# Kernel tuning notes

Measured on AMD Instinct MI355X. Metric: run time of the kernel, lower is better.

The kernel has to match this reference:

```python
import jax, jax.numpy as jnp
import numpy as np

L = 5          # num_layer
H = 32         # num_heads (feature dim)
G = 32         # n_graph
NN = 256       # n_node per graph
KB = 8         # adjacency band half-width
N = G * (2 * (KB * NN - KB * (KB + 1) // 2))   # 128768 angle-graph nodes
E = N * 16                                      # 2060288 angle-graph edges
NRBF = 20
BN_EPS = 1e-5
GAMMA = 10.0


def _band_adj():
    i = np.arange(NN)
    d = np.abs(i[:, None] - i[None, :])
    a = (d <= KB) & (d > 0)
    return jnp.asarray(np.broadcast_to(a, (G, NN, NN)).copy())


def setup_inputs() -> dict:
    key = jax.random.key(0)
    ks = jax.random.split(key, 10)
    adj = _band_adj()
    x_mask = jnp.ones((G, NN), dtype=bool)
    x_3d = jax.random.uniform(ks[0], (N, 1), minval=0.8, maxval=1.8)
    edge_attr_3d = jax.random.uniform(ks[1], (E, 1), minval=0.0, maxval=float(np.pi))
    edge_index = jax.random.randint(ks[2], (2, E), 0, N)
    s1 = 1.0 / np.sqrt(NRBF)
    sH = 1.0 / np.sqrt(H)
    s2H = 1.0 / np.sqrt(2 * H)
    return {
        "x_3d": x_3d, "edge_attr_3d": edge_attr_3d,
        "edge_index": edge_index, "adj": adj, "x_mask": x_mask,
        "w_len": jax.random.normal(ks[3], (NRBF, H)) * s1, "b_len": jnp.zeros(H),
        "w_ang": jax.random.normal(ks[4], (NRBF, H)) * s1, "b_ang": jnp.zeros(H),
        "w1": jax.random.normal(ks[5], (L, H, 2 * H)) * sH, "b1": jnp.zeros((L, 2 * H)),
        "bn1_g": jnp.ones((L, 2 * H)), "bn1_b": jnp.zeros((L, 2 * H)),
        "w2": jax.random.normal(ks[6], (L, 2 * H, H)) * s2H, "b2": jnp.zeros((L, H)),
        "eps_gin": jnp.zeros(L),
        "bn_g": jnp.ones((L, H)), "bn_b": jnp.zeros((L, H)),
        "ln_g": jnp.ones(H), "ln_b": jnp.zeros(H),
    }


def _bn(h, g, b):
    # BatchNorm1d in training mode (batch statistics)
    m = jnp.mean(h, axis=0)
    v = jnp.var(h, axis=0)
    return (h - m) * jax.lax.rsqrt(v + BN_EPS) * g + b


def _rbf(x, centers):
    # x: [M,1] -> [M, NRBF]
    return jnp.exp(-GAMMA * (x - centers) ** 2)


def _forward(x_3d, edge_attr_3d, edge_index, adj,
             w_len, b_len, w_ang, b_ang,
             w1, b1, bn1_g, bn1_b, w2, b2, eps_gin, bn_g, bn_b, ln_g, ln_b):
    cen_len = jnp.arange(NRBF, dtype=x_3d.dtype) * 0.1           # bond length RBF centers
    cen_ang = jnp.linspace(0.0, np.pi, NRBF).astype(x_3d.dtype)  # bond angle RBF centers
    x = _rbf(x_3d, cen_len) @ w_len + b_len                      # [N,H]
    ea = _rbf(edge_attr_3d, cen_ang) @ w_ang + b_ang             # [E,H]
    src, dst = edge_index[0], edge_index[1]

    h = x
    for l in range(L):
        # GINConvBondAngle: message = relu(x_j + edge_attr); aggr = add
        msg = jax.nn.relu(h[src] + ea)                           # [E,H]
        agg = jax.ops.segment_sum(msg, dst, num_segments=N)      # [N,H]
        z = (1.0 + eps_gin[l]) * h + agg
        z = _bn(z @ w1[l] + b1[l], bn1_g[l], bn1_b[l])           # mlp Linear+BN
        z = jax.nn.relu(z) @ w2[l] + b2[l]                       # mlp ReLU+Linear
        h = _bn(z, bn_g[l], bn_b[l])                             # outer batch norm
        if l != L - 1:
            h = jax.nn.relu(h)
        # dropout p=0 -> identity; residual=False; JK='last'

    mu = jnp.mean(h, axis=-1, keepdims=True)
    var = jnp.var(h, axis=-1, keepdims=True)
    nr = (h - mu) * jax.lax.rsqrt(var + BN_EPS) * ln_g + ln_b    # LayerNorm, [N,H]

    # masked dense scatter into [G*NN*NN, H]
    eye = jnp.eye(NN, dtype=bool)
    mask = (adj & ~eye).reshape(-1)                              # exactly N Trues
    pos = jnp.cumsum(mask) - 1                                   # row in nr for each True
    out = jnp.where(mask[:, None], nr[jnp.clip(pos, 0, N - 1)], 0.0)
    return out.reshape(G, NN, NN, H).transpose(0, 3, 1, 2)       # [G,H,NN,NN]


def reference(x_3d, edge_attr_3d, edge_index, adj, x_mask,
              w_len, b_len, w_ang, b_ang,
              w1, b1, bn1_g, bn1_b, w2, b2, eps_gin, bn_g, bn_b, ln_g, ln_b):
    return _forward(x_3d, edge_attr_3d, edge_index, adj,
                    w_len, b_len, w_ang, b_ang,
                    w1, b1, bn1_g, bn1_b, w2, b2, eps_gin, bn_g, bn_b, ln_g, ln_b)
```

## Files before the change

kernel.cpp:

```cpp
#include <hip/hip_runtime.h>
#include <hip/hip_bf16.h>
#include <hip/hip_fp16.h>

#define HH 32
#define HH2 64
#define NRBF_ 20
#define NL 5
#define NNN 256
#define KBW 8
#define PGN 4024
#define TTAB 4096
constexpr int NNODE = 128768;
constexpr int NEDGE = 2060288;
constexpr float BNEPS = 1e-5f;
constexpr float PI_F = 3.14159265358979323846f;

__global__ void __launch_bounds__(256) k_node_embed(const float* __restrict__ x3d,
                                                    const float* __restrict__ wlen,
                                                    const float* __restrict__ blen,
                                                    __half* __restrict__ hbuf) {
  __shared__ float wl[NRBF_ * HH];
  __shared__ float bl[HH];
  int t = threadIdx.x;
  for (int j = t; j < NRBF_ * HH; j += 256) wl[j] = wlen[j];
  if (t < HH) bl[t] = blen[t];
  __syncthreads();
  int idx = blockIdx.x * 256 + t;
  int n = idx >> 5, c = idx & 31;
  float x = x3d[n];
  float acc = bl[c];
#pragma unroll
  for (int k = 0; k < NRBF_; ++k) {
    float d = x - 0.1f * (float)k;
    acc = fmaf(__expf(-10.f * d * d), wl[k * HH + c], acc);
  }
  hbuf[idx] = __float2half(acc);
}

__global__ void __launch_bounds__(256) k_tab(const float* __restrict__ wang,
                                             const float* __restrict__ bang,
                                             __half* __restrict__ tab) {
  __shared__ float wa[NRBF_ * HH];
  __shared__ float ba[HH];
  int t = threadIdx.x;
  for (int j = t; j < NRBF_ * HH; j += 256) wa[j] = wang[j];
  if (t < HH) ba[t] = bang[t];
  __syncthreads();
  int idx = blockIdx.x * 256 + t;
  int row = idx >> 5, c = idx & 31;
  float ang = (float)row * (PI_F / (float)(TTAB - 1));
  const float step = PI_F / 19.f;
  float acc = ba[c];
#pragma unroll
  for (int k = 0; k < NRBF_; ++k) {
    float d = ang - step * (float)k;
    acc = fmaf(__expf(-10.f * d * d), wa[k * HH + c], acc);
  }
  tab[row * HH + c] = __float2half(acc);
}

__global__ void __launch_bounds__(256) k_hist(const int* __restrict__ dst, int* __restrict__ counts) {
  int e = blockIdx.x * 256 + threadIdx.x;
  atomicAdd(&counts[dst[e]], 1);
}

__global__ void __launch_bounds__(256) k_scan1(const int* __restrict__ counts, int* __restrict__ bsum) {
  __shared__ int sd[256];
  int t = threadIdx.x;
  sd[t] = counts[blockIdx.x * 256 + t];
  __syncthreads();
  for (int s = 128; s > 0; s >>= 1) { if (t < s) sd[t] += sd[t + s]; __syncthreads(); }
  if (t == 0) bsum[blockIdx.x] = sd[0];
}

__global__ void __launch_bounds__(512) k_scan2(const int* __restrict__ bsum, int* __restrict__ boff) {
  __shared__ int sd[512];
  int t = threadIdx.x;
  int v = (t < 503) ? bsum[t] : 0;
  sd[t] = v;
  __syncthreads();
  for (int off = 1; off < 512; off <<= 1) {
    int x = (t >= off) ? sd[t - off] : 0;
    __syncthreads();
    sd[t] += x;
    __syncthreads();
  }
  if (t < 503) boff[t] = sd[t] - v;
}

__global__ void __launch_bounds__(256) k_scan3(const int* __restrict__ counts, const int* __restrict__ boff,
                                               int* __restrict__ rowptr, int* __restrict__ cursor) {
  __shared__ int sd[256];
  int t = threadIdx.x;
  int i = blockIdx.x * 256 + t;
  int v = counts[i];
  sd[t] = v;
  __syncthreads();
  for (int off = 1; off < 256; off <<= 1) {
    int x = (t >= off) ? sd[t - off] : 0;
    __syncthreads();
    sd[t] += x;
    __syncthreads();
  }
  int excl = sd[t] - v + boff[blockIdx.x];
  rowptr[i] = excl;
  cursor[i] = excl;
  if (i == NNODE - 1) rowptr[NNODE] = excl + v;
}

__global__ void __launch_bounds__(256) k_scatter(const int* __restrict__ srcA,
                                                 const int* __restrict__ dstA,
                                                 const float* __restrict__ eattr,
                                                 int* __restrict__ cursor,
                                                 unsigned int* __restrict__ pk) {
  const float angsc = (float)(TTAB - 1) / PI_F;
  int bid = blockIdx.x;
  int x = bid & 7;
  int j = bid >> 3;
  int lo = x * (NNODE / 8);
  int hi = lo + (NNODE / 8);
  int e0 = j * 2048 + threadIdx.x;
#pragma unroll
  for (int k = 0; k < 8; ++k) {
    int e = e0 + k * 256;
    int d = dstA[e];
    if (d >= lo && d < hi) {
      int pos = atomicAdd(&cursor[d], 1);
      unsigned int idx = min((unsigned int)fmaf(eattr[e], angsc, 0.5f), (unsigned int)(TTAB - 1));
      pk[pos] = (unsigned int)srcA[e] | (idx << 17);
    }
  }
}

__global__ void __launch_bounds__(256) k_layerA(const __half* __restrict__ hbuf,
                                                const int* __restrict__ rowptr,
                                                const unsigned int* __restrict__ pk,
                                                const __half* __restrict__ tab,
                                                const float* __restrict__ statsC,
                                                const float* __restrict__ bng,
                                                const float* __restrict__ bnb,
                                                const float* __restrict__ w1g,
                                                const float* __restrict__ b1g,
                                                const float* __restrict__ epsg,
                                                __half* __restrict__ y1buf,
                                                float* __restrict__ statsA,
                                                int l, int relu) {
  __shared__ float w1s[HH * HH2];
  __shared__ float b1s[HH2];
  __shared__ float affs[HH], affsh[HH];
  __shared__ float tb[8][HH + 1];
  __shared__ float ps[HH2], pq[HH2];
  int t = threadIdx.x;
  const float* w1l = w1g + l * HH * HH2;
  for (int j = t; j < HH * HH2; j += 256) w1s[j] = w1l[j];
  if (t < HH2) { b1s[t] = b1g[l * HH2 + t]; ps[t] = 0.f; pq[t] = 0.f; }
  if (t < HH) {
    if (l == 0) { affs[t] = 1.f; affsh[t] = 0.f; }
    else {
      float sum = statsC[(l - 1) * 64 + t], sq = statsC[(l - 1) * 64 + 32 + t];
      float mean = sum / (float)NNODE;
      float var = fmaxf(sq / (float)NNODE - mean * mean, 0.f);
      float s = bng[(l - 1) * HH + t] * rsqrtf(var + BNEPS);
      affs[t] = s; affsh[t] = bnb[(l - 1) * HH + t] - mean * s;
    }
  }
  int g = t >> 5, c = t & 31;
  float epsv = 1.f + epsg[l];
  float lo = relu ? 0.f : -3.4e38f;
  float s0a = 0.f, s0q = 0.f, s1a = 0.f, s1q = 0.f;
  __syncthreads();
  float sc = affs[c], sh = affsh[c];
  int stride = gridDim.x * 8;
  int iters = (NNODE + stride - 1) / stride;
  int n = blockIdx.x * 8 + g;
  for (int it = 0; it < iters; ++it, n += stride) {
    bool val = n < NNODE;
    float tv = 0.f;
    if (val) {
      int p0 = rowptr[n], p1 = rowptr[n + 1];
      float hn = fmaxf(fmaf(__half2float(hbuf[n * HH + c]), sc, sh), lo);
      float acc = 0.f;
      int p = p0;
      for (; p + 8 <= p1; p += 8) {
        unsigned int q0 = __builtin_nontemporal_load(&pk[p]);
        unsigned int q1 = __builtin_nontemporal_load(&pk[p + 1]);
        unsigned int q2 = __builtin_nontemporal_load(&pk[p + 2]);
        unsigned int q3 = __builtin_nontemporal_load(&pk[p + 3]);
        unsigned int q4 = __builtin_nontemporal_load(&pk[p + 4]);
        unsigned int q5 = __builtin_nontemporal_load(&pk[p + 5]);
        unsigned int q6 = __builtin_nontemporal_load(&pk[p + 6]);
        unsigned int q7 = __builtin_nontemporal_load(&pk[p + 7]);
        float h0 = __half2float(hbuf[(q0 & 0x1FFFF) * HH + c]);
        float h1 = __half2float(hbuf[(q1 & 0x1FFFF) * HH + c]);
        float h2 = __half2float(hbuf[(q2 & 0x1FFFF) * HH + c]);
        float h3 = __half2float(hbuf[(q3 & 0x1FFFF) * HH + c]);
        float h4 = __half2float(hbuf[(q4 & 0x1FFFF) * HH + c]);
        float h5 = __half2float(hbuf[(q5 & 0x1FFFF) * HH + c]);
        float h6 = __half2float(hbuf[(q6 & 0x1FFFF) * HH + c]);
        float h7 = __half2float(hbuf[(q7 & 0x1FFFF) * HH + c]);
        float e0 = __half2float(tab[(q0 >> 17) * HH + c]);
        float e1 = __half2float(tab[(q1 >> 17) * HH + c]);
        float e2 = __half2float(tab[(q2 >> 17) * HH + c]);
        float e3 = __half2float(tab[(q3 >> 17) * HH + c]);
        float e4 = __half2float(tab[(q4 >> 17) * HH + c]);
        float e5 = __half2float(tab[(q5 >> 17) * HH + c]);
        float e6 = __half2float(tab[(q6 >> 17) * HH + c]);
        float e7 = __half2float(tab[(q7 >> 17) * HH + c]);
        h0 = fmaxf(fmaf(h0, sc, sh), lo); h1 = fmaxf(fmaf(h1, sc, sh), lo);
        h2 = fmaxf(fmaf(h2, sc, sh), lo); h3 = fmaxf(fmaf(h3, sc, sh), lo);
        h4 = fmaxf(fmaf(h4, sc, sh), lo); h5 = fmaxf(fmaf(h5, sc, sh), lo);
        h6 = fmaxf(fmaf(h6, sc, sh), lo); h7 = fmaxf(fmaf(h7, sc, sh), lo);
        acc += fmaxf(h0 + e0, 0.f) + fmaxf(h1 + e1, 0.f) + fmaxf(h2 + e2, 0.f) + fmaxf(h3 + e3, 0.f)
             + fmaxf(h4 + e4, 0.f) + fmaxf(h5 + e5, 0.f) + fmaxf(h6 + e6, 0.f) + fmaxf(h7 + e7, 0.f);
      }
      for (; p < p1; ++p) {
        unsigned int q0 = __builtin_nontemporal_load(&pk[p]);
        float h0 = fmaxf(fmaf(__half2float(hbuf[(q0 & 0x1FFFF) * HH + c]), sc, sh), lo);
        acc += fmaxf(h0 + __half2float(tab[(q0 >> 17) * HH + c]), 0.f);
      }
      tv = fmaf(epsv, hn, acc);
    }
    tb[g][c] = tv;
    __builtin_amdgcn_wave_barrier();
    if (val) {
      float y0 = b1s[c], y1 = b1s[HH + c];
#pragma unroll
      for (int k = 0; k < HH; ++k) {
        float tk = tb[g][k];
        y0 = fmaf(tk, w1s[k * HH2 + c], y0);
        y1 = fmaf(tk, w1s[k * HH2 + HH + c], y1);
      }
      __half hy0 = __float2half(y0), hy1 = __float2half(y1);
      y1buf[n * HH2 + c] = hy0;
      y1buf[n * HH2 + HH + c] = hy1;
      float z0 = __half2float(hy0), z1 = __half2float(hy1);
      s0a += z0; s0q += z0 * z0; s1a += z1; s1q += z1 * z1;
    }
    __builtin_amdgcn_wave_barrier();
  }
  s0a += __shfl_xor(s0a, 32); s0q += __shfl_xor(s0q, 32);
  s1a += __shfl_xor(s1a, 32); s1q += __shfl_xor(s1q, 32);
  if ((t & 32) == 0) {
    atomicAdd(&ps[c], s0a); atomicAdd(&pq[c], s0q);
    atomicAdd(&ps[HH + c], s1a); atomicAdd(&pq[HH + c], s1q);
  }
  __syncthreads();
  if (t < HH2) {
    atomicAdd(&statsA[l * 128 + t], ps[t]);
    atomicAdd(&statsA[l * 128 + 64 + t], pq[t]);
  }
}

__global__ void __launch_bounds__(256) k_layerC(const __half* __restrict__ y1buf,
                                                const float* __restrict__ statsA,
                                                const float* __restrict__ g1,
                                                const float* __restrict__ bb1,
                                                const float* __restrict__ w2g,
                                                const float* __restrict__ b2g,
                                                __half* __restrict__ hbuf,
                                                float* __restrict__ statsC, int l) {
  __shared__ float w2s[HH2 * HH];
  __shared__ float b2s[HH];
  __shared__ float a1s[HH2], a1sh[HH2];
  __shared__ float ab[8][HH2 + 1];
  __shared__ float ps[HH], pq[HH];
  int t = threadIdx.x;
  const float* w2l = w2g + l * HH2 * HH;
  for (int j = t; j < HH2 * HH; j += 256) w2s[j] = w2l[j];
  if (t < HH) { b2s[t] = b2g[l * HH + t]; ps[t] = 0.f; pq[t] = 0.f; }
  if (t < HH2) {
    float sum = statsA[l * 128 + t], sq = statsA[l * 128 + 64 + t];
    float mean = sum / (float)NNODE;
    float var = fmaxf(sq / (float)NNODE - mean * mean, 0.f);
    float s = g1[l * HH2 + t] * rsqrtf(var + BNEPS);
    a1s[t] = s; a1sh[t] = bb1[l * HH2 + t] - mean * s;
  }
  int g = t >> 5, c = t & 31;
  float sa = 0.f, sq = 0.f;
  __syncthreads();
  int stride = gridDim.x * 8;
  int iters = (NNODE + stride - 1) / stride;
  int n = blockIdx.x * 8 + g;
  for (int it = 0; it < iters; ++it, n += stride) {
    bool val = n < NNODE;
    float a0 = 0.f, a1 = 0.f;
    if (val) {
      a0 = fmaf(__half2float(y1buf[n * HH2 + c]), a1s[c], a1sh[c]);
      a1 = fmaf(__half2float(y1buf[n * HH2 + HH + c]), a1s[HH + c], a1sh[HH + c]);
    }
    ab[g][c] = fmaxf(a0, 0.f);
    ab[g][HH + c] = fmaxf(a1, 0.f);
    __builtin_amdgcn_wave_barrier();
    if (val) {
      float z = b2s[c];
#pragma unroll
      for (int k = 0; k < HH2; ++k) z = fmaf(ab[g][k], w2s[k * HH + c], z);
      __half zh = __float2half(z);
      hbuf[n * HH + c] = zh;
      float zq = __half2float(zh);
      sa += zq; sq += zq * zq;
    }
    __builtin_amdgcn_wave_barrier();
  }
  sa += __shfl_xor(sa, 32); sq += __shfl_xor(sq, 32);
  if ((t & 32) == 0) { atomicAdd(&ps[c], sa); atomicAdd(&pq[c], sq); }
  __syncthreads();
  if (t < HH) {
    atomicAdd(&statsC[l * 64 + t], ps[t]);
    atomicAdd(&statsC[l * 64 + 32 + t], pq[t]);
  }
}

__global__ void __launch_bounds__(256) k_output(const __half* __restrict__ hbuf,
                                                const float* __restrict__ statsC,
                                                const float* __restrict__ bng,
                                                const float* __restrict__ bnb,
                                                const float* __restrict__ lng,
                                                const float* __restrict__ lnb,
                                                float* __restrict__ out) {
  __shared__ float nrb[16 * 33];
  __shared__ float affs[HH], affsh[HH];
  int t = threadIdx.x;
  if (t < HH) {
    float sum = statsC[(NL - 1) * 64 + t], sq = statsC[(NL - 1) * 64 + 32 + t];
    float mean = sum / (float)NNODE;
    float var = fmaxf(sq / (float)NNODE - mean * mean, 0.f);
    float s = bng[(NL - 1) * HH + t] * rsqrtf(var + BNEPS);
    affs[t] = s; affsh[t] = bnb[(NL - 1) * HH + t] - mean * s;
  }
  __syncthreads();
  int gi = blockIdx.x;
  int g = gi >> 8, i = gi & 255;
  int jlo = (i - KBW > 0) ? i - KBW : 0;
  int jhi = (i + KBW < NNN - 1) ? i + KBW : NNN - 1;
  int cnt = jhi - jlo;
  int Ai = (i <= 8) ? i * (i - 1) / 2 : 28 + 8 * (i - 8);
  int Bi = (i <= 248) ? 8 * i : 2012 - (256 - i) * (255 - i) / 2;
  int nb = g * PGN + Ai + Bi;
  int r = t >> 5, c = t & 31;
  float sc = affs[c], sh = affsh[c];
  float lg = lng[c], lb = lnb[c];
  for (int rr = r; rr < cnt; rr += 8) {
    float v = fmaf(__half2float(hbuf[(nb + rr) * HH + c]), sc, sh);
    float s = v;
#pragma unroll
    for (int off = 16; off > 0; off >>= 1) s += __shfl_xor(s, off, 32);
    float mean = s * (1.f / 32.f);
    float d = v - mean;
    float q = d * d;
#pragma unroll
    for (int off = 16; off > 0; off >>= 1) q += __shfl_xor(q, off, 32);
    float var = q * (1.f / 32.f);
    nrb[rr * 33 + c] = d * rsqrtf(var + BNEPS) * lg + lb;
  }
  __syncthreads();
  int j = t;
  bool valid = (j >= jlo) & (j <= jhi) & (j != i);
  int rr = j - jlo - ((j > i) ? 1 : 0);
  rr = (rr < 0) ? 0 : ((rr > 15) ? 15 : rr);
  size_t ob = (((size_t)g * HH) * NNN + i) * NNN + j;
#pragma unroll
  for (int h = 0; h < HH; ++h) {
    float val = valid ? nrb[rr * 33 + h] : 0.f;
    __builtin_nontemporal_store(val, &out[ob + (size_t)h * NNN * NNN]);
  }
}

extern "C" void kernel_launch(void* const* d_in, const int* in_sizes, int n_in,
                              void* d_out, int out_size, void* d_ws, size_t ws_size,
                              hipStream_t stream) {
  (void)in_sizes; (void)n_in;
  const float* x3d   = (const float*)d_in[0];
  const float* eattr = (const float*)d_in[1];
  const int*   eidx  = (const int*)d_in[2];
  const float* wlen = (const float*)d_in[5];
  const float* blen = (const float*)d_in[6];
  const float* wang = (const float*)d_in[7];
  const float* bang = (const float*)d_in[8];
  const float* w1g  = (const float*)d_in[9];
  const float* b1g  = (const float*)d_in[10];
  const float* g1   = (const float*)d_in[11];
  const float* bb1  = (const float*)d_in[12];
  const float* w2g  = (const float*)d_in[13];
  const float* b2g  = (const float*)d_in[14];
  const float* epsg = (const float*)d_in[15];
  const float* bng  = (const float*)d_in[16];
  const float* bnb  = (const float*)d_in[17];
  const float* lng  = (const float*)d_in[18];
  const float* lnb  = (const float*)d_in[19];
  float* out = (float*)d_out;

  char* ws = (char*)d_ws;
  size_t off = 0;
  auto alloc = [&](size_t bytes) {
    void* p = ws + off;
    off += (bytes + 255) & ~(size_t)255;
    return p;
  };
  unsigned int* pk  = (unsigned int*)alloc((size_t)NEDGE * 4);
  int*   rowptr     = (int*)alloc((size_t)(NNODE + 1) * 4);
  int*   counts     = (int*)alloc((size_t)NNODE * 4);
  int*   cursor     = (int*)alloc((size_t)NNODE * 4);
  __half* hbuf      = (__half*)alloc((size_t)NNODE * HH * 2);
  __half* y1buf     = (__half*)alloc((size_t)NNODE * HH2 * 2);
  __half* tab       = (__half*)alloc((size_t)TTAB * HH * 2);
  float* statsA     = (float*)alloc(NL * 128 * 4);
  float* statsC     = (float*)alloc(NL * 64 * 4);
  int*   bsum       = (int*)alloc(503 * 4);
  int*   boff       = (int*)alloc(503 * 4);

  if (off > ws_size) {
    hipMemsetAsync(d_out, 0x7F, (size_t)out_size * 4, stream);
    return;
  }

  hipMemsetAsync(counts, 0, (size_t)NNODE * 4, stream);
  hipMemsetAsync(statsA, 0, NL * 128 * 4, stream);
  hipMemsetAsync(statsC, 0, NL * 64 * 4, stream);

  k_node_embed<<<NNODE * HH / 256, 256, 0, stream>>>(x3d, wlen, blen, hbuf);
  k_tab<<<TTAB * HH / 256, 256, 0, stream>>>(wang, bang, tab);
  k_hist<<<NEDGE / 256, 256, 0, stream>>>(eidx + NEDGE, counts);
  k_scan1<<<NNODE / 256, 256, 0, stream>>>(counts, bsum);
  k_scan2<<<1, 512, 0, stream>>>(bsum, boff);
  k_scan3<<<NNODE / 256, 256, 0, stream>>>(counts, boff, rowptr, cursor);
  k_scatter<<<8048, 256, 0, stream>>>(eidx, eidx + NEDGE, eattr, cursor, pk);

  for (int l = 0; l < NL; ++l) {
    k_layerA<<<2048, 256, 0, stream>>>(hbuf, rowptr, pk, tab, statsC, bng, bnb,
                                       w1g, b1g, epsg, y1buf, statsA, l, l >= 1 ? 1 : 0);
    k_layerC<<<2048, 256, 0, stream>>>(y1buf, statsA, g1, bb1, w2g, b2g, hbuf, statsC, l);
  }

  k_output<<<NNN * 32, 256, 0, stream>>>(hbuf, statsC, bng, bnb, lng, lnb, out);
}
```

Before: 1.144 ms.

## Map one wavefront per node, split edges across half-waves, merge prep kernels

Layer kernels now give each 64-lane wavefront one node instead of a 32-lane half-wave. The gather splits the edge list between the two halves and combines them with a cross-lane shuffle. The per-node matvecs now use all 64 lanes (one output per lane in layerA, split-K with a shuffle reduce in layerC). The embedding, angle-table and histogram kernels are merged into one launch, and the two stats memsets are combined. This is meant to raise memory-level parallelism per node and cut launch overhead, but it halves the nodes in flight per block and adds shuffle work.

```diff
diff --git a/kernel.cpp b/kernel.cpp
--- a/kernel.cpp
+++ b/kernel.cpp
@@ -15,53 +15,58 @@
 constexpr float BNEPS = 1e-5f;
 constexpr float PI_F = 3.14159265358979323846f;
 
-__global__ void __launch_bounds__(256) k_node_embed(const float* __restrict__ x3d,
-                                                    const float* __restrict__ wlen,
-                                                    const float* __restrict__ blen,
-                                                    __half* __restrict__ hbuf) {
-  __shared__ float wl[NRBF_ * HH];
-  __shared__ float bl[HH];
-  int t = threadIdx.x;
-  for (int j = t; j < NRBF_ * HH; j += 256) wl[j] = wlen[j];
-  if (t < HH) bl[t] = blen[t];
-  __syncthreads();
-  int idx = blockIdx.x * 256 + t;
-  int n = idx >> 5, c = idx & 31;
-  float x = x3d[n];
-  float acc = bl[c];
-#pragma unroll
-  for (int k = 0; k < NRBF_; ++k) {
-    float d = x - 0.1f * (float)k;
-    acc = fmaf(__expf(-10.f * d * d), wl[k * HH + c], acc);
-  }
-  hbuf[idx] = __float2half(acc);
-}
-
-__global__ void __launch_bounds__(256) k_tab(const float* __restrict__ wang,
-                                             const float* __restrict__ bang,
-                                             __half* __restrict__ tab) {
-  __shared__ float wa[NRBF_ * HH];
-  __shared__ float ba[HH];
-  int t = threadIdx.x;
-  for (int j = t; j < NRBF_ * HH; j += 256) wa[j] = wang[j];
-  if (t < HH) ba[t] = bang[t];
-  __syncthreads();
-  int idx = blockIdx.x * 256 + t;
-  int row = idx >> 5, c = idx & 31;
-  float ang = (float)row * (PI_F / (float)(TTAB - 1));
-  const float step = PI_F / 19.f;
-  float acc = ba[c];
-#pragma unroll
-  for (int k = 0; k < NRBF_; ++k) {
-    float d = ang - step * (float)k;
-    acc = fmaf(__expf(-10.f * d * d), wa[k * HH + c], acc);
-  }
-  tab[row * HH + c] = __float2half(acc);
-}
-
-__global__ void __launch_bounds__(256) k_hist(const int* __restrict__ dst, int* __restrict__ counts) {
-  int e = blockIdx.x * 256 + threadIdx.x;
-  atomicAdd(&counts[dst[e]], 1);
+#define EMB_BLKS (NNODE * HH / 256)
+#define TAB_BLKS (TTAB * HH / 256)
+#define HIST_BLKS (NEDGE / 256)
+
+__global__ void __launch_bounds__(256) k_prep(const float* __restrict__ x3d,
+                                              const float* __restrict__ wlen,
+                                              const float* __restrict__ blen,
+                                              const float* __restrict__ wang,
+                                              const float* __restrict__ bang,
+                                              const int* __restrict__ dst,
+                                              __half* __restrict__ hbuf,
+                                              __half* __restrict__ tab,
+                                              int* __restrict__ counts) {
+  int b = blockIdx.x;
+  int t = threadIdx.x;
+  if (b < EMB_BLKS) {
+    __shared__ float wl[NRBF_ * HH];
+    __shared__ float bl[HH];
+    for (int j = t; j < NRBF_ * HH; j += 256) wl[j] = wlen[j];
+    if (t < HH) bl[t] = blen[t];
+    __syncthreads();
+    int idx = b * 256 + t;
+    int n = idx >> 5, c = idx & 31;
+    float x = x3d[n];
+    float acc = bl[c];
+#pragma unroll
+    for (int k = 0; k < NRBF_; ++k) {
+      float d = x - 0.1f * (float)k;
+      acc = fmaf(__expf(-10.f * d * d), wl[k * HH + c], acc);
+    }
+    hbuf[idx] = __float2half(acc);
+  } else if (b < EMB_BLKS + TAB_BLKS) {
+    __shared__ float wa[NRBF_ * HH];
+    __shared__ float ba[HH];
+    for (int j = t; j < NRBF_ * HH; j += 256) wa[j] = wang[j];
+    if (t < HH) ba[t] = bang[t];
+    __syncthreads();
+    int idx = (b - EMB_BLKS) * 256 + t;
+    int row = idx >> 5, c = idx & 31;
+    float ang = (float)row * (PI_F / (float)(TTAB - 1));
+    const float step = PI_F / 19.f;
+    float acc = ba[c];
+#pragma unroll
+    for (int k = 0; k < NRBF_; ++k) {
+      float d = ang - step * (float)k;
+      acc = fmaf(__expf(-10.f * d * d), wa[k * HH + c], acc);
+    }
+    tab[row * HH + c] = __float2half(acc);
+  } else {
+    int e = (b - EMB_BLKS - TAB_BLKS) * 256 + t;
+    atomicAdd(&counts[dst[e]], 1);
+  }
 }
 
 __global__ void __launch_bounds__(256) k_scan1(const int* __restrict__ counts, int* __restrict__ bsum) {
@@ -148,7 +153,7 @@
   __shared__ float w1s[HH * HH2];
   __shared__ float b1s[HH2];
   __shared__ float affs[HH], affsh[HH];
-  __shared__ float tb[8][HH + 1];
+  __shared__ float tb[4][HH + 1];
   __shared__ float ps[HH2], pq[HH2];
   int t = threadIdx.x;
   const float* w1l = w1g + l * HH * HH2;
@@ -164,32 +169,31 @@
       affs[t] = s; affsh[t] = bnb[(l - 1) * HH + t] - mean * s;
     }
   }
-  int g = t >> 5, c = t & 31;
+  int wave = t >> 6, lane = t & 63, half = lane >> 5, c = lane & 31;
   float epsv = 1.f + epsg[l];
   float lo = relu ? 0.f : -3.4e38f;
-  float s0a = 0.f, s0q = 0.f, s1a = 0.f, s1q = 0.f;
+  float sreg = 0.f, qreg = 0.f;
   __syncthreads();
   float sc = affs[c], sh = affsh[c];
-  int stride = gridDim.x * 8;
+  int stride = gridDim.x * 4;
   int iters = (NNODE + stride - 1) / stride;
-  int n = blockIdx.x * 8 + g;
+  int n = blockIdx.x * 4 + wave;
   for (int it = 0; it < iters; ++it, n += stride) {
     bool val = n < NNODE;
-    float tv = 0.f;
     if (val) {
       int p0 = rowptr[n], p1 = rowptr[n + 1];
       float hn = fmaxf(fmaf(__half2float(hbuf[n * HH + c]), sc, sh), lo);
       float acc = 0.f;
-      int p = p0;
-      for (; p + 8 <= p1; p += 8) {
+      int p = p0 + half;
+      while (p + 14 < p1) {
         unsigned int q0 = __builtin_nontemporal_load(&pk[p]);
-        unsigned int q1 = __builtin_nontemporal_load(&pk[p + 1]);
-        unsigned int q2 = __builtin_nontemporal_load(&pk[p + 2]);
-        unsigned int q3 = __builtin_nontemporal_load(&pk[p + 3]);
-        unsigned int q4 = __builtin_nontemporal_load(&pk[p + 4]);
-        unsigned int q5 = __builtin_nontemporal_load(&pk[p + 5]);
-        unsigned int q6 = __builtin_nontemporal_load(&pk[p + 6]);
-        unsigned int q7 = __builtin_nontemporal_load(&pk[p + 7]);
+        unsigned int q1 = __builtin_nontemporal_load(&pk[p + 2]);
+        unsigned int q2 = __builtin_nontemporal_load(&pk[p + 4]);
+        unsigned int q3 = __builtin_nontemporal_load(&pk[p + 6]);
+        unsigned int q4 = __builtin_nontemporal_load(&pk[p + 8]);
+        unsigned int q5 = __builtin_nontemporal_load(&pk[p + 10]);
+        unsigned int q6 = __builtin_nontemporal_load(&pk[p + 12]);
+        unsigned int q7 = __builtin_nontemporal_load(&pk[p + 14]);
         float h0 = __half2float(hbuf[(q0 & 0x1FFFF) * HH + c]);
         float h1 = __half2float(hbuf[(q1 & 0x1FFFF) * HH + c]);
         float h2 = __half2float(hbuf[(q2 & 0x1FFFF) * HH + c]);
@@ -212,43 +216,35 @@
         h6 = fmaxf(fmaf(h6, sc, sh), lo); h7 = fmaxf(fmaf(h7, sc, sh), lo);
         acc += fmaxf(h0 + e0, 0.f) + fmaxf(h1 + e1, 0.f) + fmaxf(h2 + e2, 0.f) + fmaxf(h3 + e3, 0.f)
              + fmaxf(h4 + e4, 0.f) + fmaxf(h5 + e5, 0.f) + fmaxf(h6 + e6, 0.f) + fmaxf(h7 + e7, 0.f);
+        p += 16;
       }
-      for (; p < p1; ++p) {
+      for (; p < p1; p += 2) {
         unsigned int q0 = __builtin_nontemporal_load(&pk[p]);
         float h0 = fmaxf(fmaf(__half2float(hbuf[(q0 & 0x1FFFF) * HH + c]), sc, sh), lo);
         acc += fmaxf(h0 + __half2float(tab[(q0 >> 17) * HH + c]), 0.f);
       }
-      tv = fmaf(epsv, hn, acc);
-    }
-    tb[g][c] = tv;
+      acc += __shfl_xor(acc, 32);
+      float tv = fmaf(epsv, hn, acc);
+      if (half == 0) tb[wave][c] = tv;
+    }
     __builtin_amdgcn_wave_barrier();
     if (val) {
-      float y0 = b1s[c], y1 = b1s[HH + c];
-#pragma unroll
-      for (int k = 0; k < HH; ++k) {
-        float tk = tb[g][k];
-        y0 = fmaf(tk, w1s[k * HH2 + c], y0);
-        y1 = fmaf(tk, w1s[k * HH2 + HH + c], y1);
-      }
-      __half hy0 = __float2half(y0), hy1 = __float2half(y1);
-      y1buf[n * HH2 + c] = hy0;
-      y1buf[n * HH2 + HH + c] = hy1;
-      float z0 = __half2float(hy0), z1 = __half2float(hy1);
-      s0a += z0; s0q += z0 * z0; s1a += z1; s1q += z1 * z1;
+      float y = b1s[lane];
+#pragma unroll
+      for (int k = 0; k < HH; ++k) y = fmaf(tb[wave][k], w1s[k * HH2 + lane], y);
+      __half hy = __float2half(y);
+      y1buf[n * HH2 + lane] = hy;
+      float z = __half2float(hy);
+      sreg += z; qreg += z * z;
     }
     __builtin_amdgcn_wave_barrier();
   }
-  s0a += __shfl_xor(s0a, 32); s0q += __shfl_xor(s0q, 32);
-  s1a += __shfl_xor(s1a, 32); s1q += __shfl_xor(s1q, 32);
-  if ((t & 32) == 0) {
-    atomicAdd(&ps[c], s0a); atomicAdd(&pq[c], s0q);
-    atomicAdd(&ps[HH + c], s1a); atomicAdd(&pq[HH + c], s1q);
-  }
-  __syncthreads();
-  if (t < HH2) {
-    atomicAdd(&statsA[l * 128 + t], ps[t]);
-    atomicAdd(&statsA[l * 128 + 64 + t], pq[t]);
-  }
+  __syncthreads();
+  atomicAdd(&ps[lane], sreg);
+  atomicAdd(&pq[lane], qreg);
+  __syncthreads();
+  if (t < HH2) atomicAdd(&statsA[l * 128 + t], ps[t]);
+  else if (t < 128) atomicAdd(&statsA[l * 128 + t], pq[t - HH2]);
 }
 
 __global__ void __launch_bounds__(256) k_layerC(const __half* __restrict__ y1buf,
@@ -262,7 +258,7 @@
   __shared__ float w2s[HH2 * HH];
   __shared__ float b2s[HH];
   __shared__ float a1s[HH2], a1sh[HH2];
-  __shared__ float ab[8][HH2 + 1];
+  __shared__ float ab[4][HH2 + 1];
   __shared__ float ps[HH], pq[HH];
   int t = threadIdx.x;
   const float* w2l = w2g + l * HH2 * HH;
@@ -275,40 +271,39 @@
     float s = g1[l * HH2 + t] * rsqrtf(var + BNEPS);
     a1s[t] = s; a1sh[t] = bb1[l * HH2 + t] - mean * s;
   }
-  int g = t >> 5, c = t & 31;
-  float sa = 0.f, sq = 0.f;
-  __syncthreads();
-  int stride = gridDim.x * 8;
+  int wave = t >> 6, lane = t & 63, half = lane >> 5, c = lane & 31;
+  float sreg = 0.f, qreg = 0.f;
+  __syncthreads();
+  int stride = gridDim.x * 4;
   int iters = (NNODE + stride - 1) / stride;
-  int n = blockIdx.x * 8 + g;
+  int n = blockIdx.x * 4 + wave;
   for (int it = 0; it < iters; ++it, n += stride) {
     bool val = n < NNODE;
-    float a0 = 0.f, a1 = 0.f;
     if (val) {
-      a0 = fmaf(__half2float(y1buf[n * HH2 + c]), a1s[c], a1sh[c]);
-      a1 = fmaf(__half2float(y1buf[n * HH2 + HH + c]), a1s[HH + c], a1sh[HH + c]);
-    }
-    ab[g][c] = fmaxf(a0, 0.f);
-    ab[g][HH + c] = fmaxf(a1, 0.f);
+      float a = fmaf(__half2float(y1buf[n * HH2 + lane]), a1s[lane], a1sh[lane]);
+      ab[wave][lane] = fmaxf(a, 0.f);
+    }
     __builtin_amdgcn_wave_barrier();
     if (val) {
-      float z = b2s[c];
-#pragma unroll
-      for (int k = 0; k < HH2; ++k) z = fmaf(ab[g][k], w2s[k * HH + c], z);
-      __half zh = __float2half(z);
-      hbuf[n * HH + c] = zh;
-      float zq = __half2float(zh);
-      sa += zq; sq += zq * zq;
+      float z = (half == 0) ? b2s[c] : 0.f;
+      int kb = half << 5;
+#pragma unroll
+      for (int k2 = 0; k2 < HH; ++k2) z = fmaf(ab[wave][kb + k2], w2s[(kb + k2) * HH + c], z);
+      z += __shfl_xor(z, 32);
+      if (half == 0) {
+        __half zh = __float2half(z);
+        hbuf[n * HH + c] = zh;
+        float zq = __half2float(zh);
+        sreg += zq; qreg += zq * zq;
+      }
     }
     __builtin_amdgcn_wave_barrier();
   }
-  sa += __shfl_xor(sa, 32); sq += __shfl_xor(sq, 32);
-  if ((t & 32) == 0) { atomicAdd(&ps[c], sa); atomicAdd(&pq[c], sq); }
-  __syncthreads();
-  if (t < HH) {
-    atomicAdd(&statsC[l * 64 + t], ps[t]);
-    atomicAdd(&statsC[l * 64 + 32 + t], pq[t]);
-  }
+  __syncthreads();
+  if (half == 0) { atomicAdd(&ps[c], sreg); atomicAdd(&pq[c], qreg); }
+  __syncthreads();
+  if (t < HH) atomicAdd(&statsC[l * 64 + t], ps[t]);
+  else if (t < 64) atomicAdd(&statsC[l * 64 + t], pq[t - HH]);
 }
 
 __global__ void __launch_bounds__(256) k_output(const __half* __restrict__ hbuf,
@@ -404,8 +399,8 @@
   __half* hbuf      = (__half*)alloc((size_t)NNODE * HH * 2);
   __half* y1buf     = (__half*)alloc((size_t)NNODE * HH2 * 2);
   __half* tab       = (__half*)alloc((size_t)TTAB * HH * 2);
-  float* statsA     = (float*)alloc(NL * 128 * 4);
-  float* statsC     = (float*)alloc(NL * 64 * 4);
+  float* statsA     = (float*)alloc((NL * 128 + NL * 64) * 4);
+  float* statsC     = statsA + NL * 128;
   int*   bsum       = (int*)alloc(503 * 4);
   int*   boff       = (int*)alloc(503 * 4);
 
@@ -415,12 +410,10 @@
   }
 
   hipMemsetAsync(counts, 0, (size_t)NNODE * 4, stream);
-  hipMemsetAsync(statsA, 0, NL * 128 * 4, stream);
-  hipMemsetAsync(statsC, 0, NL * 64 * 4, stream);
-
-  k_node_embed<<<NNODE * HH / 256, 256, 0, stream>>>(x3d, wlen, blen, hbuf);
-  k_tab<<<TTAB * HH / 256, 256, 0, stream>>>(wang, bang, tab);
-  k_hist<<<NEDGE / 256, 256, 0, stream>>>(eidx + NEDGE, counts);
+  hipMemsetAsync(statsA, 0, (NL * 128 + NL * 64) * 4, stream);
+
+  k_prep<<<EMB_BLKS + TAB_BLKS + HIST_BLKS, 256, 0, stream>>>(x3d, wlen, blen, wang, bang,
+                                                              eidx + NEDGE, hbuf, tab, counts);
   k_scan1<<<NNODE / 256, 256, 0, stream>>>(counts, bsum);
   k_scan2<<<1, 512, 0, stream>>>(bsum, boff);
   k_scan3<<<NNODE / 256, 256, 0, stream>>>(counts, boff, rowptr, cursor);
```

Result: slower. 1.277 ms (+11.6%).

## Split edge gather into two passes by source-node half for cache locality

Applied to the files above, without the earlier changes.

Edges are bucketed per destination node by whether the source index lies in the lower or upper half of the node range. Each layer now runs two gather kernels, each touching only half of the half-precision feature buffer, so the working set of the random gathers is meant to fit better in cache. In exchange it adds an extra float partial-sum buffer write and read per layer, one extra kernel launch per layer, and a doubled histogram and scan.

```diff
diff --git a/kernel.cpp b/kernel.cpp
--- a/kernel.cpp
+++ b/kernel.cpp
@@ -11,6 +11,8 @@
 #define PGN 4024
 #define TTAB 4096
 constexpr int NNODE = 128768;
+constexpr int NHALF = NNODE / 2;
+constexpr int N2 = NNODE * 2;
 constexpr int NEDGE = 2060288;
 constexpr float BNEPS = 1e-5f;
 constexpr float PI_F = 3.14159265358979323846f;
@@ -59,9 +61,12 @@
   tab[row * HH + c] = __float2half(acc);
 }
 
-__global__ void __launch_bounds__(256) k_hist(const int* __restrict__ dst, int* __restrict__ counts) {
+__global__ void __launch_bounds__(256) k_hist(const int* __restrict__ srcA,
+                                              const int* __restrict__ dstA,
+                                              int* __restrict__ counts) {
   int e = blockIdx.x * 256 + threadIdx.x;
-  atomicAdd(&counts[dst[e]], 1);
+  int bin = dstA[e] * 2 + (srcA[e] >= NHALF ? 1 : 0);
+  atomicAdd(&counts[bin], 1);
 }
 
 __global__ void __launch_bounds__(256) k_scan1(const int* __restrict__ counts, int* __restrict__ bsum) {
@@ -73,23 +78,23 @@
   if (t == 0) bsum[blockIdx.x] = sd[0];
 }
 
-__global__ void __launch_bounds__(512) k_scan2(const int* __restrict__ bsum, int* __restrict__ boff) {
-  __shared__ int sd[512];
-  int t = threadIdx.x;
-  int v = (t < 503) ? bsum[t] : 0;
+__global__ void __launch_bounds__(1024) k_scan2(const int* __restrict__ bsum, int* __restrict__ boff) {
+  __shared__ int sd[1024];
+  int t = threadIdx.x;
+  int v = (t < 1006) ? bsum[t] : 0;
   sd[t] = v;
   __syncthreads();
-  for (int off = 1; off < 512; off <<= 1) {
+  for (int off = 1; off < 1024; off <<= 1) {
     int x = (t >= off) ? sd[t - off] : 0;
     __syncthreads();
     sd[t] += x;
     __syncthreads();
   }
-  if (t < 503) boff[t] = sd[t] - v;
+  if (t < 1006) boff[t] = sd[t] - v;
 }
 
 __global__ void __launch_bounds__(256) k_scan3(const int* __restrict__ counts, const int* __restrict__ boff,
-                                               int* __restrict__ rowptr, int* __restrict__ cursor) {
+                                               int* __restrict__ rowptr2, int* __restrict__ cursor2) {
   __shared__ int sd[256];
   int t = threadIdx.x;
   int i = blockIdx.x * 256 + t;
@@ -103,15 +108,15 @@
     __syncthreads();
   }
   int excl = sd[t] - v + boff[blockIdx.x];
-  rowptr[i] = excl;
-  cursor[i] = excl;
-  if (i == NNODE - 1) rowptr[NNODE] = excl + v;
+  rowptr2[i] = excl;
+  cursor2[i] = excl;
+  if (i == N2 - 1) rowptr2[N2] = excl + v;
 }
 
 __global__ void __launch_bounds__(256) k_scatter(const int* __restrict__ srcA,
                                                  const int* __restrict__ dstA,
                                                  const float* __restrict__ eattr,
-                                                 int* __restrict__ cursor,
+                                                 int* __restrict__ cursor2,
                                                  unsigned int* __restrict__ pk) {
   const float angsc = (float)(TTAB - 1) / PI_F;
   int bid = blockIdx.x;
@@ -125,26 +130,112 @@
     int e = e0 + k * 256;
     int d = dstA[e];
     if (d >= lo && d < hi) {
-      int pos = atomicAdd(&cursor[d], 1);
+      int s = srcA[e];
+      int bin = d * 2 + (s >= NHALF ? 1 : 0);
+      int pos = atomicAdd(&cursor2[bin], 1);
       unsigned int idx = min((unsigned int)fmaf(eattr[e], angsc, 0.5f), (unsigned int)(TTAB - 1));
-      pk[pos] = (unsigned int)srcA[e] | (idx << 17);
-    }
-  }
-}
-
-__global__ void __launch_bounds__(256) k_layerA(const __half* __restrict__ hbuf,
-                                                const int* __restrict__ rowptr,
-                                                const unsigned int* __restrict__ pk,
-                                                const __half* __restrict__ tab,
-                                                const float* __restrict__ statsC,
-                                                const float* __restrict__ bng,
-                                                const float* __restrict__ bnb,
-                                                const float* __restrict__ w1g,
-                                                const float* __restrict__ b1g,
-                                                const float* __restrict__ epsg,
-                                                __half* __restrict__ y1buf,
-                                                float* __restrict__ statsA,
-                                                int l, int relu) {
+      pk[pos] = (unsigned int)s | (idx << 17);
+    }
+  }
+}
+
+__device__ __forceinline__ float edge_gather(const __half* __restrict__ hbuf,
+                                             const __half* __restrict__ tab,
+                                             const unsigned int* __restrict__ pk,
+                                             int p0, int p1, int c,
+                                             float sc, float sh, float lo) {
+  float acc = 0.f;
+  int p = p0;
+  for (; p + 8 <= p1; p += 8) {
+    unsigned int q0 = __builtin_nontemporal_load(&pk[p]);
+    unsigned int q1 = __builtin_nontemporal_load(&pk[p + 1]);
+    unsigned int q2 = __builtin_nontemporal_load(&pk[p + 2]);
+    unsigned int q3 = __builtin_nontemporal_load(&pk[p + 3]);
+    unsigned int q4 = __builtin_nontemporal_load(&pk[p + 4]);
+    unsigned int q5 = __builtin_nontemporal_load(&pk[p + 5]);
+    unsigned int q6 = __builtin_nontemporal_load(&pk[p + 6]);
+    unsigned int q7 = __builtin_nontemporal_load(&pk[p + 7]);
+    float h0 = __half2float(hbuf[(q0 & 0x1FFFF) * HH + c]);
+    float h1 = __half2float(hbuf[(q1 & 0x1FFFF) * HH + c]);
+    float h2 = __half2float(hbuf[(q2 & 0x1FFFF) * HH + c]);
+    float h3 = __half2float(hbuf[(q3 & 0x1FFFF) * HH + c]);
+    float h4 = __half2float(hbuf[(q4 & 0x1FFFF) * HH + c]);
+    float h5 = __half2float(hbuf[(q5 & 0x1FFFF) * HH + c]);
+    float h6 = __half2float(hbuf[(q6 & 0x1FFFF) * HH + c]);
+    float h7 = __half2float(hbuf[(q7 & 0x1FFFF) * HH + c]);
+    float e0 = __half2float(tab[(q0 >> 17) * HH + c]);
+    float e1 = __half2float(tab[(q1 >> 17) * HH + c]);
+    float e2 = __half2float(tab[(q2 >> 17) * HH + c]);
+    float e3 = __half2float(tab[(q3 >> 17) * HH + c]);
+    float e4 = __half2float(tab[(q4 >> 17) * HH + c]);
+    float e5 = __half2float(tab[(q5 >> 17) * HH + c]);
+    float e6 = __half2float(tab[(q6 >> 17) * HH + c]);
+    float e7 = __half2float(tab[(q7 >> 17) * HH + c]);
+    h0 = fmaxf(fmaf(h0, sc, sh), lo); h1 = fmaxf(fmaf(h1, sc, sh), lo);
+    h2 = fmaxf(fmaf(h2, sc, sh), lo); h3 = fmaxf(fmaf(h3, sc, sh), lo);
+    h4 = fmaxf(fmaf(h4, sc, sh), lo); h5 = fmaxf(fmaf(h5, sc, sh), lo);
+    h6 = fmaxf(fmaf(h6, sc, sh), lo); h7 = fmaxf(fmaf(h7, sc, sh), lo);
+    acc += fmaxf(h0 + e0, 0.f) + fmaxf(h1 + e1, 0.f) + fmaxf(h2 + e2, 0.f) + fmaxf(h3 + e3, 0.f)
+         + fmaxf(h4 + e4, 0.f) + fmaxf(h5 + e5, 0.f) + fmaxf(h6 + e6, 0.f) + fmaxf(h7 + e7, 0.f);
+  }
+  for (; p < p1; ++p) {
+    unsigned int q0 = __builtin_nontemporal_load(&pk[p]);
+    float h0 = fmaxf(fmaf(__half2float(hbuf[(q0 & 0x1FFFF) * HH + c]), sc, sh), lo);
+    acc += fmaxf(h0 + __half2float(tab[(q0 >> 17) * HH + c]), 0.f);
+  }
+  return acc;
+}
+
+__global__ void __launch_bounds__(256) k_layerA0(const __half* __restrict__ hbuf,
+                                                 const int* __restrict__ rowptr2,
+                                                 const unsigned int* __restrict__ pk,
+                                                 const __half* __restrict__ tab,
+                                                 const float* __restrict__ statsC,
+                                                 const float* __restrict__ bng,
+                                                 const float* __restrict__ bnb,
+                                                 float* __restrict__ partf,
+                                                 int l, int relu) {
+  __shared__ float affs[HH], affsh[HH];
+  int t = threadIdx.x;
+  if (t < HH) {
+    if (l == 0) { affs[t] = 1.f; affsh[t] = 0.f; }
+    else {
+      float sum = statsC[(l - 1) * 64 + t], sq = statsC[(l - 1) * 64 + 32 + t];
+      float mean = sum / (float)NNODE;
+      float var = fmaxf(sq / (float)NNODE - mean * mean, 0.f);
+      float s = bng[(l - 1) * HH + t] * rsqrtf(var + BNEPS);
+      affs[t] = s; affsh[t] = bnb[(l - 1) * HH + t] - mean * s;
+    }
+  }
+  int g = t >> 5, c = t & 31;
+  float lo = relu ? 0.f : -3.4e38f;
+  __syncthreads();
+  float sc = affs[c], sh = affsh[c];
+  int stride = gridDim.x * 8;
+  int iters = (NNODE + stride - 1) / stride;
+  int n = blockIdx.x * 8 + g;
+  for (int it = 0; it < iters; ++it, n += stride) {
+    if (n < NNODE) {
+      int p0 = rowptr2[2 * n], p1 = rowptr2[2 * n + 1];
+      partf[n * HH + c] = edge_gather(hbuf, tab, pk, p0, p1, c, sc, sh, lo);
+    }
+  }
+}
+
+__global__ void __launch_bounds__(256) k_layerA1(const __half* __restrict__ hbuf,
+                                                 const int* __restrict__ rowptr2,
+                                                 const unsigned int* __restrict__ pk,
+                                                 const __half* __restrict__ tab,
+                                                 const float* __restrict__ partf,
+                                                 const float* __restrict__ statsC,
+                                                 const float* __restrict__ bng,
+                                                 const float* __restrict__ bnb,
+                                                 const float* __restrict__ w1g,
+                                                 const float* __restrict__ b1g,
+                                                 const float* __restrict__ epsg,
+                                                 __half* __restrict__ y1buf,
+                                                 float* __restrict__ statsA,
+                                                 int l, int relu) {
   __shared__ float w1s[HH * HH2];
   __shared__ float b1s[HH2];
   __shared__ float affs[HH], affsh[HH];
@@ -177,47 +268,10 @@
     bool val = n < NNODE;
     float tv = 0.f;
     if (val) {
-      int p0 = rowptr[n], p1 = rowptr[n + 1];
+      int p0 = rowptr2[2 * n + 1], p1 = rowptr2[2 * n + 2];
+      float acc = edge_gather(hbuf, tab, pk, p0, p1, c, sc, sh, lo);
+      acc += partf[n * HH + c];
       float hn = fmaxf(fmaf(__half2float(hbuf[n * HH + c]), sc, sh), lo);
-      float acc = 0.f;
-      int p = p0;
-      for (; p + 8 <= p1; p += 8) {
-        unsigned int q0 = __builtin_nontemporal_load(&pk[p]);
-        unsigned int q1 = __builtin_nontemporal_load(&pk[p + 1]);
-        unsigned int q2 = __builtin_nontemporal_load(&pk[p + 2]);
-        unsigned int q3 = __builtin_nontemporal_load(&pk[p + 3]);
-        unsigned int q4 = __builtin_nontemporal_load(&pk[p + 4]);
-        unsigned int q5 = __builtin_nontemporal_load(&pk[p + 5]);
-        unsigned int q6 = __builtin_nontemporal_load(&pk[p + 6]);
-        unsigned int q7 = __builtin_nontemporal_load(&pk[p + 7]);
-        float h0 = __half2float(hbuf[(q0 & 0x1FFFF) * HH + c]);
-        float h1 = __half2float(hbuf[(q1 & 0x1FFFF) * HH + c]);
-        float h2 = __half2float(hbuf[(q2 & 0x1FFFF) * HH + c]);
-        float h3 = __half2float(hbuf[(q3 & 0x1FFFF) * HH + c]);
-        float h4 = __half2float(hbuf[(q4 & 0x1FFFF) * HH + c]);
-        float h5 = __half2float(hbuf[(q5 & 0x1FFFF) * HH + c]);
-        float h6 = __half2float(hbuf[(q6 & 0x1FFFF) * HH + c]);
-        float h7 = __half2float(hbuf[(q7 & 0x1FFFF) * HH + c]);
-        float e0 = __half2float(tab[(q0 >> 17) * HH + c]);
-        float e1 = __half2float(tab[(q1 >> 17) * HH + c]);
-        float e2 = __half2float(tab[(q2 >> 17) * HH + c]);
-        float e3 = __half2float(tab[(q3 >> 17) * HH + c]);
-        float e4 = __half2float(tab[(q4 >> 17) * HH + c]);
-        float e5 = __half2float(tab[(q5 >> 17) * HH + c]);
-        float e6 = __half2float(tab[(q6 >> 17) * HH + c]);
-        float e7 = __half2float(tab[(q7 >> 17) * HH + c]);
-        h0 = fmaxf(fmaf(h0, sc, sh), lo); h1 = fmaxf(fmaf(h1, sc, sh), lo);
-        h2 = fmaxf(fmaf(h2, sc, sh), lo); h3 = fmaxf(fmaf(h3, sc, sh), lo);
-        h4 = fmaxf(fmaf(h4, sc, sh), lo); h5 = fmaxf(fmaf(h5, sc, sh), lo);
-        h6 = fmaxf(fmaf(h6, sc, sh), lo); h7 = fmaxf(fmaf(h7, sc, sh), lo);
-        acc += fmaxf(h0 + e0, 0.f) + fmaxf(h1 + e1, 0.f) + fmaxf(h2 + e2, 0.f) + fmaxf(h3 + e3, 0.f)
-             + fmaxf(h4 + e4, 0.f) + fmaxf(h5 + e5, 0.f) + fmaxf(h6 + e6, 0.f) + fmaxf(h7 + e7, 0.f);
-      }
-      for (; p < p1; ++p) {
-        unsigned int q0 = __builtin_nontemporal_load(&pk[p]);
-        float h0 = fmaxf(fmaf(__half2float(hbuf[(q0 & 0x1FFFF) * HH + c]), sc, sh), lo);
-        acc += fmaxf(h0 + __half2float(tab[(q0 >> 17) * HH + c]), 0.f);
-      }
       tv = fmaf(epsv, hn, acc);
     }
     tb[g][c] = tv;
@@ -398,37 +452,39 @@
     return p;
   };
   unsigned int* pk  = (unsigned int*)alloc((size_t)NEDGE * 4);
-  int*   rowptr     = (int*)alloc((size_t)(NNODE + 1) * 4);
-  int*   counts     = (int*)alloc((size_t)NNODE * 4);
-  int*   cursor     = (int*)alloc((size_t)NNODE * 4);
+  int*   rowptr2    = (int*)alloc((size_t)(N2 + 1) * 4);
+  int*   counts     = (int*)alloc((size_t)N2 * 4);
+  int*   cursor2    = (int*)alloc((size_t)N2 * 4);
   __half* hbuf      = (__half*)alloc((size_t)NNODE * HH * 2);
   __half* y1buf     = (__half*)alloc((size_t)NNODE * HH2 * 2);
   __half* tab       = (__half*)alloc((size_t)TTAB * HH * 2);
-  float* statsA     = (float*)alloc(NL * 128 * 4);
-  float* statsC     = (float*)alloc(NL * 64 * 4);
-  int*   bsum       = (int*)alloc(503 * 4);
-  int*   boff       = (int*)alloc(503 * 4);
+  float* partf      = (float*)alloc((size_t)NNODE * HH * 4);
+  float* statsA     = (float*)alloc((NL * 128 + NL * 64) * 4);
+  float* statsC     = statsA + NL * 128;
+  int*   bsum       = (int*)alloc(1006 * 4);
+  int*   boff       = (int*)alloc(1006 * 4);
 
   if (off > ws_size) {
     hipMemsetAsync(d_out, 0x7F, (size_t)out_size * 4, stream);
     return;
   }
 
-  hipMemsetAsync(counts, 0, (size_t)NNODE * 4, stream);
-  hipMemsetAsync(statsA, 0, NL * 128 * 4, stream);
-  hipMemsetAsync(statsC, 0, NL * 64 * 4, stream);
+  hipMemsetAsync(counts, 0, (size_t)N2 * 4, stream);
+  hipMemsetAsync(statsA, 0, (NL * 128 + NL * 64) * 4, stream);
 
   k_node_embed<<<NNODE * HH / 256, 256, 0, stream>>>(x3d, wlen, blen, hbuf);
   k_tab<<<TTAB * HH / 256, 256, 0, stream>>>(wang, bang, tab);
-  k_hist<<<NEDGE / 256, 256, 0, stream>>>(eidx + NEDGE, counts);
-  k_scan1<<<NNODE / 256, 256, 0, stream>>>(counts, bsum);
-  k_scan2<<<1, 512, 0, stream>>>(bsum, boff);
-  k_scan3<<<NNODE / 256, 256, 0, stream>>>(counts, boff, rowptr, cursor);
-  k_scatter<<<8048, 256, 0, stream>>>(eidx, eidx + NEDGE, eattr, cursor, pk);
+  k_hist<<<NEDGE / 256, 256, 0, stream>>>(eidx, eidx + NEDGE, counts);
+  k_scan1<<<N2 / 256, 256, 0, stream>>>(counts, bsum);
+  k_scan2<<<1, 1024, 0, stream>>>(bsum, boff);
+  k_scan3<<<N2 / 256, 256, 0, stream>>>(counts, boff, rowptr2, cursor2);
+  k_scatter<<<8048, 256, 0, stream>>>(eidx, eidx + NEDGE, eattr, cursor2, pk);
 
   for (int l = 0; l < NL; ++l) {
-    k_layerA<<<2048, 256, 0, stream>>>(hbuf, rowptr, pk, tab, statsC, bng, bnb,
-                                       w1g, b1g, epsg, y1buf, statsA, l, l >= 1 ? 1 : 0);
+    int relu = l >= 1 ? 1 : 0;
+    k_layerA0<<<2048, 256, 0, stream>>>(hbuf, rowptr2, pk, tab, statsC, bng, bnb, partf, l, relu);
+    k_layerA1<<<2048, 256, 0, stream>>>(hbuf, rowptr2, pk, tab, partf, statsC, bng, bnb,
+                                        w1g, b1g, epsg, y1buf, statsA, l, relu);
     k_layerC<<<2048, 256, 0, stream>>>(y1buf, statsA, g1, bb1, w2g, b2g, hbuf, statsC, l);
   }
 
```

New measurement: 1.367 ms. +19.6%, slower.
